# Kernel tuning notes

Hardware: AMD Instinct MI355X
Metric: run time of the kernel (lower is better)

## Reference

```python
import jax, jax.numpy as jnp
import numpy as np

LSH_NUM_PROJS = 7
BLOCK_SIZE = 256      # key block size
SAMPLE_SIZE = 256
B, H, N, D = 1, 32, 8192, 128


def _gray_perm(num_projs):
    # AngularLSH._unit_hamming_distance_array: Gray-code bucket permutation
    a = np.array([0, 1], dtype=np.int32)
    for _ in range(num_projs - 1):
        a = np.concatenate([a, np.flip(a) + a.shape[0]])
    return jnp.asarray(a)


def _lsh_hash(x, proj_dir, perm):
    # x: [B,H,N,D], proj_dir: [D,R] -> bucket ids [B,H,N]
    bits = jnp.einsum('bhnd,dr->bhnr', x, proj_dir) > 0
    enc = 2 ** jnp.arange(proj_dir.shape[-1], dtype=jnp.int32)
    bin_ids = jnp.sum(bits.astype(jnp.int32) * enc, axis=-1)
    return perm[bin_ids]


def _attn_lse(q, k, v, scale, bias=None):
    # exact attention returning output and log-sum-exp of scaled scores
    s = jnp.einsum('...qd,...kd->...qk', q, k) * scale
    if bias is not None:
        s = s + bias
    m = jnp.max(s, axis=-1, keepdims=True)
    p = jnp.exp(s - m)
    denom = jnp.sum(p, axis=-1, keepdims=True)
    attn = jnp.einsum('...qk,...kd->...qd', p, v) / denom
    lse = m + jnp.log(denom)  # [..., q, 1]
    return attn, lse


def _take(x, idx):
    # gather along the sequence axis (dim 2); idx: [B,H,M]
    return jnp.take_along_axis(x, idx[..., None], axis=2)


def hyper_attention(q, k, v, proj_dir, sampled_set):
    b, h, n, d = q.shape
    scale = d ** -0.5
    perm = _gray_perm(LSH_NUM_PROJS)
    # 1) sortLSH: sort q and k by angular-LSH bucket (stable)
    q_idx = jnp.argsort(_lsh_hash(q, proj_dir, perm), axis=2)
    k_idx = jnp.argsort(_lsh_hash(k, proj_dir, perm), axis=2)
    q_idx_inv = jnp.argsort(q_idx, axis=2)
    q_s = _take(q, q_idx)
    k_s = _take(k, k_idx)
    v_s = _take(v, k_idx)
    nb = n // BLOCK_SIZE          # number of key blocks
    qbs = n // nb                 # query block size
    # block-diagonal exact attention in sorted order
    qb = q_s.reshape(b, h, nb, qbs, d)
    kb = k_s.reshape(b, h, nb, BLOCK_SIZE, d)
    vb = v_s.reshape(b, h, nb, BLOCK_SIZE, d)
    attn_blk, lse_blk = _attn_lse(qb, kb, vb, scale)
    attn_blk = attn_blk.reshape(b, h, n, d)
    lse_blk = lse_blk.reshape(b, h, n, 1)
    attn_blk = _take(attn_blk, q_idx_inv)
    lse_blk = _take(lse_blk, q_idx_inv)
    # 2) residual: uniform sampling of keys (indices into sorted key order)
    s_size = sampled_set.shape[-1]
    k_sub = _take(k_s, sampled_set)   # [B,H,S,D]
    v_sub = _take(v_s, sampled_set)
    # mask out samples falling in the query's own diagonal block
    same_block = (jnp.arange(n)[None, None, :, None] // qbs) == (sampled_set[:, :, None, :] // BLOCK_SIZE)
    bias = jnp.where(same_block, jnp.finfo(q.dtype).min, 0.0).astype(q.dtype)
    attn_res, lse_res = _attn_lse(q_s, k_sub, v_sub, scale, bias=bias)
    lse_res = lse_res + jnp.log(n / s_size)  # importance weight n_key/sample_size
    attn_res = _take(attn_res, q_idx_inv)
    lse_res = _take(lse_res, q_idx_inv)
    # 3) combine estimators: softmax-weighted average in log space
    lse = jnp.logaddexp(lse_blk, lse_res)
    return jnp.exp(lse_blk - lse) * attn_blk + jnp.exp(lse_res - lse) * attn_res


def setup_inputs() -> dict:
    key = jax.random.key(0)
    k1, k2, k3, k4, k5 = jax.random.split(key, 5)
    return {
        'queries': jax.random.normal(k1, (B, H, N, D), dtype=jnp.float32),
        'keys': jax.random.normal(k2, (B, H, N, D), dtype=jnp.float32),
        'vals': jax.random.normal(k3, (B, H, N, D), dtype=jnp.float32),
        'proj_dir': jax.random.normal(k4, (D, LSH_NUM_PROJS), dtype=jnp.float32),
        'sampled_set': jax.random.randint(k5, (B, H, SAMPLE_SIZE), 0, N),
    }


def reference(queries, keys, vals, proj_dir, sampled_set):
    return hyper_attention(queries, keys, vals, proj_dir, sampled_set)
```

## Files before the change

kernel.cpp:

```cpp
#include <hip/hip_runtime.h>
#include <hip/hip_bf16.h>
#include <math.h>

#define Hh 32
#define Nseq 8192
#define Dh 128
#define NBd 32
#define BLKSZ 256
#define SAMP 256
#define CHK 64
#define LOG32 3.4657359027997265f
#define SCALE 0.088388347648318447f
#define SKW 136
#define SVB 264

typedef float f32x4 __attribute__((ext_vector_type(4)));
typedef unsigned ui32x4 __attribute__((ext_vector_type(4)));
typedef __bf16 bf16x8 __attribute__((ext_vector_type(8)));

__device__ __forceinline__ f32x4 mfma16(bf16x8 a, bf16x8 b, f32x4 c) {
  return __builtin_amdgcn_mfma_f32_16x16x32_bf16(a, b, c, 0, 0, 0);
}

__device__ __forceinline__ bf16x8 cvt8(const float* __restrict__ p) {
  float4 a = ((const float4*)p)[0];
  float4 b = ((const float4*)p)[1];
  bf16x8 r;
  r[0] = (__bf16)a.x; r[1] = (__bf16)a.y; r[2] = (__bf16)a.z; r[3] = (__bf16)a.w;
  r[4] = (__bf16)b.x; r[5] = (__bf16)b.y; r[6] = (__bf16)b.z; r[7] = (__bf16)b.w;
  return r;
}

__device__ __forceinline__ bf16x8 cvt8v(float4 a, float4 b) {
  bf16x8 r;
  r[0] = (__bf16)a.x; r[1] = (__bf16)a.y; r[2] = (__bf16)a.z; r[3] = (__bf16)a.w;
  r[4] = (__bf16)b.x; r[5] = (__bf16)b.y; r[6] = (__bf16)b.z; r[7] = (__bf16)b.w;
  return r;
}

__device__ __forceinline__ unsigned pack2(float a, float b, float& ra, float& rb) {
  __bf16 ba = (__bf16)a, bb = (__bf16)b;
  ra = (float)ba; rb = (float)bb;
  return ((unsigned)__builtin_bit_cast(unsigned short, bb) << 16) |
         (unsigned)__builtin_bit_cast(unsigned short, ba);
}

__global__ __launch_bounds__(256) void lsh_hash_kernel(
    const float* __restrict__ q, const float* __restrict__ k,
    const float* __restrict__ proj, int* __restrict__ buckets) {
  int row = blockIdx.x * 256 + threadIdx.x;
  const float* x = ((row >> 18) ? k : q) + (size_t)(row & (Hh * Nseq - 1)) * Dh;
  double acc[7] = {0, 0, 0, 0, 0, 0, 0};
#pragma unroll 8
  for (int d0 = 0; d0 < Dh; d0 += 4) {
    float4 xv = *(const float4*)(x + d0);
    double x0 = (double)xv.x, x1 = (double)xv.y, x2 = (double)xv.z, x3 = (double)xv.w;
#pragma unroll
    for (int j = 0; j < 7; j++) {
      acc[j] = fma(x0, (double)proj[(d0 + 0) * 7 + j], acc[j]);
      acc[j] = fma(x1, (double)proj[(d0 + 1) * 7 + j], acc[j]);
      acc[j] = fma(x2, (double)proj[(d0 + 2) * 7 + j], acc[j]);
      acc[j] = fma(x3, (double)proj[(d0 + 3) * 7 + j], acc[j]);
    }
  }
  int bin = 0;
#pragma unroll
  for (int j = 0; j < 7; j++) bin |= (acc[j] > 0.0 ? 1 : 0) << j;
  buckets[row] = bin ^ (bin >> 1);
}

__global__ __launch_bounds__(64) void bucket_sort_kernel(
    const int* __restrict__ buckets, int* __restrict__ idx) {
  __shared__ unsigned hist[64][128];
  int t = threadIdx.x;
  int base = blockIdx.x * Nseq;
  for (int b = 0; b < 128; b++) hist[t][b] = 0;
  __syncthreads();
  for (int i = 0; i < 128; i++) {
    int b = buckets[base + t * 128 + i];
    hist[t][b]++;
  }
  __syncthreads();
  int b0 = 2 * t, b1 = 2 * t + 1;
  unsigned tot0 = 0, tot1 = 0;
  for (int tt = 0; tt < 64; tt++) { unsigned h = hist[tt][b0]; hist[tt][b0] = tot0; tot0 += h; }
  for (int tt = 0; tt < 64; tt++) { unsigned h = hist[tt][b1]; hist[tt][b1] = tot1; tot1 += h; }
  unsigned pair = tot0 + tot1;
  unsigned scan = pair;
  for (int s = 1; s < 64; s <<= 1) {
    unsigned u = __shfl_up(scan, s);
    if (t >= s) scan += u;
  }
  unsigned start0 = scan - pair;
  unsigned start1 = start0 + tot0;
  __syncthreads();
  for (int tt = 0; tt < 64; tt++) { hist[tt][b0] += start0; hist[tt][b1] += start1; }
  __syncthreads();
  for (int i = 0; i < 128; i++) {
    int gi = t * 128 + i;
    int b = buckets[base + gi];
    unsigned pos = hist[t][b]++;
    idx[base + pos] = gi;
  }
}

__global__ __launch_bounds__(512, 2) void hyper_attn_blk_kernel(
    const float* __restrict__ q, const float* __restrict__ k, const float* __restrict__ v,
    const int* __restrict__ q_idx, const int* __restrict__ k_idx,
    float* __restrict__ out, float* __restrict__ lse_ws) {
  __shared__ int s_orig[BLKSZ];
  __shared__ __attribute__((aligned(16))) __bf16 s_k[2][CHK][SKW];
  __shared__ __attribute__((aligned(16))) __bf16 s_vt[2][Dh][72];

  const int c = blockIdx.x, bh = blockIdx.y;
  const int tid = threadIdx.x;
  const int w = tid >> 6, l = tid & 63;
  const int l4 = l >> 4, lm = l & 15;
  const int jk = tid >> 3, pk = tid & 7;

  if (tid < BLKSZ) s_orig[tid] = k_idx[bh * Nseq + c * BLKSZ + tid];

  bf16x8 qf[2][4];
  const int* qi = q_idx + bh * Nseq + c * BLKSZ + w * 32;
#pragma unroll
  for (int rt = 0; rt < 2; rt++) {
    int orig = qi[rt * 16 + lm];
    const float* qp = q + ((size_t)bh * Nseq + orig) * Dh + l4 * 8;
#pragma unroll
    for (int dc = 0; dc < 4; dc++) qf[rt][dc] = cvt8(qp + dc * 32);
  }

  f32x4 O[2][8];
  float mrow[2] = {-INFINITY, -INFINITY};
  float lsum[2] = {0.f, 0.f};
#pragma unroll
  for (int rt = 0; rt < 2; rt++)
#pragma unroll
    for (int dt = 0; dt < 8; dt++) { O[rt][dt][0]=0.f; O[rt][dt][1]=0.f; O[rt][dt][2]=0.f; O[rt][dt][3]=0.f; }

  __syncthreads();

  {
    int origk = s_orig[jk];
    const float* kp = k + ((size_t)bh * Nseq + origk) * Dh + pk * 16;
    *(bf16x8*)&s_k[0][jk][pk * 16]     = cvt8(kp);
    *(bf16x8*)&s_k[0][jk][pk * 16 + 8] = cvt8(kp + 8);
    int origv = s_orig[l];
    const float* vp = v + ((size_t)bh * Nseq + origv) * Dh + w * 16;
    float4 A = ((const float4*)vp)[0], B = ((const float4*)vp)[1];
    float4 C = ((const float4*)vp)[2], Dv = ((const float4*)vp)[3];
    float tmp[16] = {A.x,A.y,A.z,A.w,B.x,B.y,B.z,B.w,C.x,C.y,C.z,C.w,Dv.x,Dv.y,Dv.z,Dv.w};
#pragma unroll
    for (int dd = 0; dd < 16; dd++) s_vt[0][w * 16 + dd][l] = (__bf16)tmp[dd];
  }
  __syncthreads();

  const int laneA = lm + 32 * (l4 & 1);
  const bool hi = (l4 >> 1) & 1;

  for (int ch = 0; ch < 4; ch++) {
    const int cur = ch & 1;
    const bool pf = (ch + 1 < 4);

    float4 kA, kB, kC, kD, vA, vB, vC, vD;
    if (pf) {
      int origk = s_orig[(ch + 1) * CHK + jk];
      const float4* kp = (const float4*)(k + ((size_t)bh * Nseq + origk) * Dh + pk * 16);
      kA = kp[0]; kB = kp[1]; kC = kp[2]; kD = kp[3];
      int origv = s_orig[(ch + 1) * CHK + l];
      const float4* vp = (const float4*)(v + ((size_t)bh * Nseq + origv) * Dh + w * 16);
      vA = vp[0]; vB = vp[1]; vC = vp[2]; vD = vp[3];
    }

    float sc[2][4][4];
#pragma unroll
    for (int ct = 0; ct < 4; ct++) {
      f32x4 acc0, acc1;
      acc0[0]=0.f;acc0[1]=0.f;acc0[2]=0.f;acc0[3]=0.f;
      acc1[0]=0.f;acc1[1]=0.f;acc1[2]=0.f;acc1[3]=0.f;
#pragma unroll
      for (int dc = 0; dc < 4; dc++) {
        bf16x8 kf = *(const bf16x8*)&s_k[cur][ct * 16 + lm][dc * 32 + l4 * 8];
        acc0 = mfma16(kf, qf[0][dc], acc0);
        acc1 = mfma16(kf, qf[1][dc], acc1);
      }
#pragma unroll
      for (int r = 0; r < 4; r++) {
        sc[0][ct][r] = acc0[r] * SCALE;
        sc[1][ct][r] = acc1[r] * SCALE;
      }
    }

    unsigned q01[2][4], q23[2][4];
#pragma unroll
    for (int rt = 0; rt < 2; rt++) {
      float mc = sc[rt][0][0];
#pragma unroll
      for (int ct = 0; ct < 4; ct++)
#pragma unroll
        for (int r = 0; r < 4; r++) mc = fmaxf(mc, sc[rt][ct][r]);
      mc = fmaxf(mc, __shfl_xor(mc, 16));
      mc = fmaxf(mc, __shfl_xor(mc, 32));
      float mn = fmaxf(mrow[rt], mc);
      float alpha = __expf(mrow[rt] - mn);
      mrow[rt] = mn;
      f32x4 aO;
#pragma unroll
      for (int r = 0; r < 4; r++) aO[r] = __shfl(alpha, l4 * 4 + r);
#pragma unroll
      for (int dt = 0; dt < 8; dt++) O[rt][dt] *= aO;
      float rsum = 0.f;
#pragma unroll
      for (int ct = 0; ct < 4; ct++) {
        float p0 = __expf(sc[rt][ct][0] - mn);
        float p1 = __expf(sc[rt][ct][1] - mn);
        float p2 = __expf(sc[rt][ct][2] - mn);
        float p3 = __expf(sc[rt][ct][3] - mn);
        float ra, rb, rc, rd;
        q01[rt][ct] = pack2(p0, p1, ra, rb);
        q23[rt][ct] = pack2(p2, p3, rc, rd);
        rsum += (ra + rb) + (rc + rd);
      }
      rsum += __shfl_xor(rsum, 16);
      rsum += __shfl_xor(rsum, 32);
      lsum[rt] = lsum[rt] * alpha + rsum;
    }

    if (pf) {
      *(bf16x8*)&s_k[cur ^ 1][jk][pk * 16]     = cvt8v(kA, kB);
      *(bf16x8*)&s_k[cur ^ 1][jk][pk * 16 + 8] = cvt8v(kC, kD);
      float ta[16] = {vA.x,vA.y,vA.z,vA.w,vB.x,vB.y,vB.z,vB.w,
                      vC.x,vC.y,vC.z,vC.w,vD.x,vD.y,vD.z,vD.w};
#pragma unroll
      for (int dd = 0; dd < 16; dd++) s_vt[cur ^ 1][w * 16 + dd][l] = (__bf16)ta[dd];
    }

#pragma unroll
    for (int kc = 0; kc < 2; kc++) {
      bf16x8 pa[2];
#pragma unroll
      for (int rt = 0; rt < 2; rt++) {
        unsigned a0 = __shfl((int)q01[rt][2 * kc],     laneA);
        unsigned b0 = __shfl((int)q01[rt][2 * kc + 1], laneA);
        unsigned a1 = __shfl((int)q23[rt][2 * kc],     laneA);
        unsigned b1 = __shfl((int)q23[rt][2 * kc + 1], laneA);
        unsigned a2 = __shfl((int)q01[rt][2 * kc],     laneA + 16);
        unsigned b2 = __shfl((int)q01[rt][2 * kc + 1], laneA + 16);
        unsigned a3 = __shfl((int)q23[rt][2 * kc],     laneA + 16);
        unsigned b3 = __shfl((int)q23[rt][2 * kc + 1], laneA + 16);
        ui32x4 pw;
        pw[0] = hi ? b0 : a0;
        pw[1] = hi ? b1 : a1;
        pw[2] = hi ? b2 : a2;
        pw[3] = hi ? b3 : a3;
        pa[rt] = __builtin_bit_cast(bf16x8, pw);
      }
#pragma unroll
      for (int dt = 0; dt < 8; dt++) {
        bf16x8 vb = *(const bf16x8*)&s_vt[cur][dt * 16 + lm][kc * 32 + l4 * 8];
        O[0][dt] = mfma16(pa[0], vb, O[0][dt]);
        O[1][dt] = mfma16(pa[1], vb, O[1][dt]);
      }
    }
    __syncthreads();
  }

#pragma unroll
  for (int rt = 0; rt < 2; rt++) {
    float inv = 1.0f / lsum[rt];
    f32x4 invr;
#pragma unroll
    for (int r = 0; r < 4; r++) invr[r] = __shfl(inv, l4 * 4 + r);
    int orow[4];
#pragma unroll
    for (int r = 0; r < 4; r++)
      orow[r] = q_idx[bh * Nseq + c * BLKSZ + w * 32 + rt * 16 + l4 * 4 + r];
#pragma unroll
    for (int r = 0; r < 4; r++) {
      float* op = out + ((size_t)bh * Nseq + orow[r]) * Dh + lm;
#pragma unroll
      for (int dt = 0; dt < 8; dt++) op[dt * 16] = O[rt][dt][r] * invr[r];
    }
    if (l4 == 0) {
      int orow0 = q_idx[bh * Nseq + c * BLKSZ + w * 32 + rt * 16 + lm];
      lse_ws[bh * Nseq + orow0] = mrow[rt] + __logf(lsum[rt]);
    }
  }
}

__global__ __launch_bounds__(512, 1) void hyper_attn_res_kernel(
    const float* __restrict__ q, const float* __restrict__ k, const float* __restrict__ v,
    const int* __restrict__ sampled, const int* __restrict__ q_idx,
    const int* __restrict__ k_idx, const float* __restrict__ lse_ws,
    float* __restrict__ out) {
  __shared__ int s_sp[SAMP];
  __shared__ __attribute__((aligned(16))) __bf16 s_k[SAMP][SKW];
  __shared__ __attribute__((aligned(16))) __bf16 s_vt[Dh][SVB];

  const int bh = blockIdx.x >> 3, oct = blockIdx.x & 7;
  const int tid = threadIdx.x;
  const int w = tid >> 6, l = tid & 63;
  const int l4 = l >> 4, lm = l & 15;
  const int jk = tid >> 3, pk = tid & 7;

  if (tid < SAMP) s_sp[tid] = sampled[bh * SAMP + tid];

#pragma unroll
  for (int ps = 0; ps < 4; ps++) {
    int key = ps * 64 + jk;
    int sp = sampled[bh * SAMP + key];
    int orig = k_idx[bh * Nseq + sp];
    const float4* kp = (const float4*)(k + ((size_t)bh * Nseq + orig) * Dh + pk * 16);
    *(bf16x8*)&s_k[key][pk * 16]     = cvt8v(kp[0], kp[1]);
    *(bf16x8*)&s_k[key][pk * 16 + 8] = cvt8v(kp[2], kp[3]);
  }
#pragma unroll
  for (int ps = 0; ps < 4; ps++) {
    int key = ps * 64 + l;
    int sp = sampled[bh * SAMP + key];
    int orig = k_idx[bh * Nseq + sp];
    const float4* vp = (const float4*)(v + ((size_t)bh * Nseq + orig) * Dh + w * 16);
    float4 A = vp[0], B = vp[1], C = vp[2], Dv = vp[3];
    float tmp[16] = {A.x,A.y,A.z,A.w,B.x,B.y,B.z,B.w,C.x,C.y,C.z,C.w,Dv.x,Dv.y,Dv.z,Dv.w};
#pragma unroll
    for (int dd = 0; dd < 16; dd++) s_vt[w * 16 + dd][key] = (__bf16)tmp[dd];
  }
  __syncthreads();

  const int laneA = lm + 32 * (l4 & 1);
  const bool hi = (l4 >> 1) & 1;

  for (int t = 0; t < 4; t++) {
    const int rowb = oct * 1024 + w * 128 + t * 32;
    const int c_tile = rowb >> 8;

    bf16x8 qf[2][4];
#pragma unroll
    for (int rt = 0; rt < 2; rt++) {
      int orig = q_idx[bh * Nseq + rowb + rt * 16 + lm];
      const float* qp = q + ((size_t)bh * Nseq + orig) * Dh + l4 * 8;
#pragma unroll
      for (int dc = 0; dc < 4; dc++) qf[rt][dc] = cvt8(qp + dc * 32);
    }

    f32x4 O[2][8];
    float mrow[2] = {-INFINITY, -INFINITY};
    float lsum[2] = {0.f, 0.f};
#pragma unroll
    for (int rt = 0; rt < 2; rt++)
#pragma unroll
      for (int dt = 0; dt < 8; dt++) { O[rt][dt][0]=0.f; O[rt][dt][1]=0.f; O[rt][dt][2]=0.f; O[rt][dt][3]=0.f; }

    for (int ch = 0; ch < 4; ch++) {
      float sc[2][4][4];
#pragma unroll
      for (int ct = 0; ct < 4; ct++) {
        f32x4 acc0, acc1;
        acc0[0]=0.f;acc0[1]=0.f;acc0[2]=0.f;acc0[3]=0.f;
        acc1[0]=0.f;acc1[1]=0.f;acc1[2]=0.f;acc1[3]=0.f;
#pragma unroll
        for (int dc = 0; dc < 4; dc++) {
          bf16x8 kf = *(const bf16x8*)&s_k[ch * 64 + ct * 16 + lm][dc * 32 + l4 * 8];
          acc0 = mfma16(kf, qf[0][dc], acc0);
          acc1 = mfma16(kf, qf[1][dc], acc1);
        }
        ui32x4 spv = *(const ui32x4*)&s_sp[ch * 64 + ct * 16 + l4 * 4];
#pragma unroll
        for (int r = 0; r < 4; r++) {
          float add = ((((int)spv[r]) >> 8) == c_tile) ? -1e38f : LOG32;
          sc[0][ct][r] = acc0[r] * SCALE + add;
          sc[1][ct][r] = acc1[r] * SCALE + add;
        }
      }

      unsigned q01[2][4], q23[2][4];
#pragma unroll
      for (int rt = 0; rt < 2; rt++) {
        float mc = sc[rt][0][0];
#pragma unroll
        for (int ct = 0; ct < 4; ct++)
#pragma unroll
          for (int r = 0; r < 4; r++) mc = fmaxf(mc, sc[rt][ct][r]);
        mc = fmaxf(mc, __shfl_xor(mc, 16));
        mc = fmaxf(mc, __shfl_xor(mc, 32));
        float mn = fmaxf(mrow[rt], mc);
        float alpha = __expf(mrow[rt] - mn);
        mrow[rt] = mn;
        f32x4 aO;
#pragma unroll
        for (int r = 0; r < 4; r++) aO[r] = __shfl(alpha, l4 * 4 + r);
#pragma unroll
        for (int dt = 0; dt < 8; dt++) O[rt][dt] *= aO;
        float rsum = 0.f;
#pragma unroll
        for (int ct = 0; ct < 4; ct++) {
          float p0 = __expf(sc[rt][ct][0] - mn);
          float p1 = __expf(sc[rt][ct][1] - mn);
          float p2 = __expf(sc[rt][ct][2] - mn);
          float p3 = __expf(sc[rt][ct][3] - mn);
          float ra, rb, rc, rd;
          q01[rt][ct] = pack2(p0, p1, ra, rb);
          q23[rt][ct] = pack2(p2, p3, rc, rd);
          rsum += (ra + rb) + (rc + rd);
        }
        rsum += __shfl_xor(rsum, 16);
        rsum += __shfl_xor(rsum, 32);
        lsum[rt] = lsum[rt] * alpha + rsum;
      }

#pragma unroll
      for (int kc = 0; kc < 2; kc++) {
        bf16x8 pa[2];
#pragma unroll
        for (int rt = 0; rt < 2; rt++) {
          unsigned a0 = __shfl((int)q01[rt][2 * kc],     laneA);
          unsigned b0 = __shfl((int)q01[rt][2 * kc + 1], laneA);
          unsigned a1 = __shfl((int)q23[rt][2 * kc],     laneA);
          unsigned b1 = __shfl((int)q23[rt][2 * kc + 1], laneA);
          unsigned a2 = __shfl((int)q01[rt][2 * kc],     laneA + 16);
          unsigned b2 = __shfl((int)q01[rt][2 * kc + 1], laneA + 16);
          unsigned a3 = __shfl((int)q23[rt][2 * kc],     laneA + 16);
          unsigned b3 = __shfl((int)q23[rt][2 * kc + 1], laneA + 16);
          ui32x4 pw;
          pw[0] = hi ? b0 : a0;
          pw[1] = hi ? b1 : a1;
          pw[2] = hi ? b2 : a2;
          pw[3] = hi ? b3 : a3;
          pa[rt] = __builtin_bit_cast(bf16x8, pw);
        }
#pragma unroll
        for (int dt = 0; dt < 8; dt++) {
          bf16x8 vb = *(const bf16x8*)&s_vt[dt * 16 + lm][ch * 64 + kc * 32 + l4 * 8];
          O[0][dt] = mfma16(pa[0], vb, O[0][dt]);
          O[1][dt] = mfma16(pa[1], vb, O[1][dt]);
        }
      }
    }

#pragma unroll
    for (int rt = 0; rt < 2; rt++) {
      float lse_r = mrow[rt] + __logf(lsum[rt]);
      float inv = 1.0f / lsum[rt];
#pragma unroll
      for (int r = 0; r < 4; r++) {
        float lrr  = __shfl(lse_r, l4 * 4 + r);
        float invr = __shfl(inv,   l4 * 4 + r);
        int orow = q_idx[bh * Nseq + rowb + rt * 16 + l4 * 4 + r];
        float lb = lse_ws[bh * Nseq + orow];
        float m2 = fmaxf(lb, lrr);
        float wb = __expf(lb - m2), wr = __expf(lrr - m2);
        float sw = 1.0f / (wb + wr);
        wb *= sw; wr *= sw;
        float* op = out + ((size_t)bh * Nseq + orow) * Dh + lm;
#pragma unroll
        for (int dt = 0; dt < 8; dt++)
          op[dt * 16] = wb * op[dt * 16] + wr * (O[rt][dt][r] * invr);
      }
    }
  }
}

extern "C" void kernel_launch(void* const* d_in, const int* in_sizes, int n_in,
                              void* d_out, int out_size, void* d_ws, size_t ws_size,
                              hipStream_t stream) {
  const float* q    = (const float*)d_in[0];
  const float* k    = (const float*)d_in[1];
  const float* v    = (const float*)d_in[2];
  const float* proj = (const float*)d_in[3];
  const int* samp   = (const int*)d_in[4];
  float* out = (float*)d_out;

  int* buckets = (int*)d_ws;
  int* idx = buckets + 2 * Hh * Nseq;
  float* lse_ws = (float*)buckets;

  lsh_hash_kernel<<<(2 * Hh * Nseq) / 256, 256, 0, stream>>>(q, k, proj, buckets);
  bucket_sort_kernel<<<2 * Hh, 64, 0, stream>>>(buckets, idx);
  hyper_attn_blk_kernel<<<dim3(NBd, Hh), 512, 0, stream>>>(
      q, k, v, idx , idx + Hh * Nseq , out, lse_ws);
  hyper_attn_res_kernel<<<8 * Hh, 512, 0, stream>>>(
      q, k, v, samp, idx , idx + Hh * Nseq , lse_ws, out);
}
```

Measured before the change: 326.3 us.

## Fuse block and residual attention into one pass over 512 keys with pre-permuted bf16 K/V

Merges the block-diagonal and sampled-residual attention into one online-softmax pass per query block. Each pass covers the 256 block keys plus the 256 sampled keys, with an additive bias applying the same-block mask and the log importance weight. This removes the LSE workspace, the second kernel and the read-modify-write combine of the output. A new permute kernel writes sorted K and transposed V (and the sampled subsets) as bf16 so the attention loop does contiguous 16-byte loads without gathers or conversion. The cost is an extra pass over K/V and more workspace, with a fallback gather kernel if the workspace is too small. The sampled K/V are also no longer reused across query tiles.

Result: no change. 324.4 us (-0.6%).

```diff
diff --git a/kernel.cpp b/kernel.cpp
--- a/kernel.cpp
+++ b/kernel.cpp
@@ -8,11 +8,13 @@
 #define NBd 32
 #define BLKSZ 256
 #define SAMP 256
+#define KVT 512
 #define CHK 64
+#define NCH 8
 #define LOG32 3.4657359027997265f
 #define SCALE 0.088388347648318447f
 #define SKW 136
-#define SVB 264
+#define SVW 72
 
 typedef float f32x4 __attribute__((ext_vector_type(4)));
 typedef unsigned ui32x4 __attribute__((ext_vector_type(4)));
@@ -104,21 +106,74 @@
   }
 }
 
-__global__ __launch_bounds__(512, 2) void hyper_attn_blk_kernel(
-    const float* __restrict__ q, const float* __restrict__ k, const float* __restrict__ v,
-    const int* __restrict__ q_idx, const int* __restrict__ k_idx,
-    float* __restrict__ out, float* __restrict__ lse_ws) {
-  __shared__ int s_orig[BLKSZ];
+__global__ __launch_bounds__(256) void permute_kernel(
+    const float* __restrict__ k, const float* __restrict__ v,
+    const int* __restrict__ k_idx, const int* __restrict__ sampled,
+    __bf16* __restrict__ K_s, __bf16* __restrict__ V_t,
+    __bf16* __restrict__ K_sp, __bf16* __restrict__ V_sp) {
+  __shared__ __attribute__((aligned(16))) __bf16 s_t[Dh][SVW];
+  const int tile = blockIdx.x, bh = blockIdx.y;
+  const int t = threadIdx.x;
+  const int j = t >> 2, seg = (t & 3) * 32;
+  const bool blk = (tile < 128);
+  int dpos, orig;
+  if (blk) {
+    dpos = tile * 64 + j;
+    orig = k_idx[bh * Nseq + dpos];
+  } else {
+    dpos = (tile - 128) * 64 + j;
+    int sp = sampled[bh * SAMP + dpos];
+    orig = k_idx[bh * Nseq + sp];
+  }
+  {
+    const float4* kp = (const float4*)(k + ((size_t)bh * Nseq + orig) * Dh + seg);
+    __bf16* dst = blk ? K_s + ((size_t)bh * Nseq + dpos) * Dh + seg
+                      : K_sp + ((size_t)bh * SAMP + dpos) * Dh + seg;
+#pragma unroll
+    for (int i = 0; i < 4; i++) *(bf16x8*)(dst + i * 8) = cvt8v(kp[2 * i], kp[2 * i + 1]);
+  }
+  {
+    const float4* vp = (const float4*)(v + ((size_t)bh * Nseq + orig) * Dh + seg);
+#pragma unroll
+    for (int i = 0; i < 8; i++) {
+      float4 a = vp[i];
+      s_t[seg + i * 4 + 0][j] = (__bf16)a.x;
+      s_t[seg + i * 4 + 1][j] = (__bf16)a.y;
+      s_t[seg + i * 4 + 2][j] = (__bf16)a.z;
+      s_t[seg + i * 4 + 3][j] = (__bf16)a.w;
+    }
+  }
+  __syncthreads();
+  {
+    int d = t >> 1, half = (t & 1) * 32;
+    __bf16* dst = blk ? V_t + ((size_t)(bh * Dh + d)) * Nseq + tile * 64 + half
+                      : V_sp + ((size_t)(bh * Dh + d)) * SAMP + (tile - 128) * 64 + half;
+    const __bf16* srcp = &s_t[d][half];
+#pragma unroll
+    for (int i = 0; i < 4; i++) *(ui32x4*)(dst + i * 8) = *(const ui32x4*)(srcp + i * 8);
+  }
+}
+
+__global__ __launch_bounds__(512, 2) void hyper_attn_kernel(
+    const float* __restrict__ q, const __bf16* __restrict__ K_s,
+    const __bf16* __restrict__ V_t, const __bf16* __restrict__ K_sp,
+    const __bf16* __restrict__ V_sp, const int* __restrict__ sampled,
+    const int* __restrict__ q_idx, float* __restrict__ out) {
+  __shared__ __attribute__((aligned(16))) float s_add[SAMP];
   __shared__ __attribute__((aligned(16))) __bf16 s_k[2][CHK][SKW];
-  __shared__ __attribute__((aligned(16))) __bf16 s_vt[2][Dh][72];
+  __shared__ __attribute__((aligned(16))) __bf16 s_vt[2][Dh][SVW];
 
   const int c = blockIdx.x, bh = blockIdx.y;
   const int tid = threadIdx.x;
   const int w = tid >> 6, l = tid & 63;
   const int l4 = l >> 4, lm = l & 15;
   const int jk = tid >> 3, pk = tid & 7;
-
-  if (tid < BLKSZ) s_orig[tid] = k_idx[bh * Nseq + c * BLKSZ + tid];
+  const int dv = tid >> 2, ks = (tid & 3) * 16;
+
+  if (tid < SAMP) {
+    int sp = sampled[bh * SAMP + tid];
+    s_add[tid] = ((sp >> 8) == c) ? -1e38f : LOG32;
+  }
 
   bf16x8 qf[2][4];
   const int* qi = q_idx + bh * Nseq + c * BLKSZ + w * 32;
@@ -141,35 +196,33 @@
   __syncthreads();
 
   {
-    int origk = s_orig[jk];
-    const float* kp = k + ((size_t)bh * Nseq + origk) * Dh + pk * 16;
-    *(bf16x8*)&s_k[0][jk][pk * 16]     = cvt8(kp);
-    *(bf16x8*)&s_k[0][jk][pk * 16 + 8] = cvt8(kp + 8);
-    int origv = s_orig[l];
-    const float* vp = v + ((size_t)bh * Nseq + origv) * Dh + w * 16;
-    float4 A = ((const float4*)vp)[0], B = ((const float4*)vp)[1];
-    float4 C = ((const float4*)vp)[2], Dv = ((const float4*)vp)[3];
-    float tmp[16] = {A.x,A.y,A.z,A.w,B.x,B.y,B.z,B.w,C.x,C.y,C.z,C.w,Dv.x,Dv.y,Dv.z,Dv.w};
-#pragma unroll
-    for (int dd = 0; dd < 16; dd++) s_vt[0][w * 16 + dd][l] = (__bf16)tmp[dd];
+    const __bf16* kp = K_s + ((size_t)(bh * Nseq + c * BLKSZ) + jk) * Dh + pk * 16;
+    *(ui32x4*)&s_k[0][jk][pk * 16]     = *(const ui32x4*)kp;
+    *(ui32x4*)&s_k[0][jk][pk * 16 + 8] = *(const ui32x4*)(kp + 8);
+    const __bf16* vp = V_t + ((size_t)(bh * Dh + dv)) * Nseq + c * BLKSZ + ks;
+    *(ui32x4*)&s_vt[0][dv][ks]     = *(const ui32x4*)vp;
+    *(ui32x4*)&s_vt[0][dv][ks + 8] = *(const ui32x4*)(vp + 8);
   }
   __syncthreads();
 
   const int laneA = lm + 32 * (l4 & 1);
   const bool hi = (l4 >> 1) & 1;
 
-  for (int ch = 0; ch < 4; ch++) {
+  for (int ch = 0; ch < NCH; ch++) {
     const int cur = ch & 1;
-    const bool pf = (ch + 1 < 4);
-
-    float4 kA, kB, kC, kD, vA, vB, vC, vD;
+    const bool pf = (ch + 1 < NCH);
+
+    ui32x4 kA, kB, vA, vB;
     if (pf) {
-      int origk = s_orig[(ch + 1) * CHK + jk];
-      const float4* kp = (const float4*)(k + ((size_t)bh * Nseq + origk) * Dh + pk * 16);
-      kA = kp[0]; kB = kp[1]; kC = kp[2]; kD = kp[3];
-      int origv = s_orig[(ch + 1) * CHK + l];
-      const float4* vp = (const float4*)(v + ((size_t)bh * Nseq + origv) * Dh + w * 16);
-      vA = vp[0]; vB = vp[1]; vC = vp[2]; vD = vp[3];
+      int cn = ch + 1;
+      const __bf16* kp = (cn < 4)
+          ? K_s + ((size_t)(bh * Nseq + c * BLKSZ + cn * CHK) + jk) * Dh + pk * 16
+          : K_sp + ((size_t)(bh * SAMP + (cn - 4) * CHK) + jk) * Dh + pk * 16;
+      kA = *(const ui32x4*)kp; kB = *(const ui32x4*)(kp + 8);
+      const __bf16* vp = (cn < 4)
+          ? V_t + ((size_t)(bh * Dh + dv)) * Nseq + c * BLKSZ + cn * CHK + ks
+          : V_sp + ((size_t)(bh * Dh + dv)) * SAMP + (cn - 4) * CHK + ks;
+      vA = *(const ui32x4*)vp; vB = *(const ui32x4*)(vp + 8);
     }
 
     float sc[2][4][4];
@@ -184,10 +237,13 @@
         acc0 = mfma16(kf, qf[0][dc], acc0);
         acc1 = mfma16(kf, qf[1][dc], acc1);
       }
+      f32x4 addv;
+      if (ch < 4) { addv[0]=0.f; addv[1]=0.f; addv[2]=0.f; addv[3]=0.f; }
+      else addv = *(const f32x4*)&s_add[(ch - 4) * CHK + ct * 16 + l4 * 4];
 #pragma unroll
       for (int r = 0; r < 4; r++) {
-        sc[0][ct][r] = acc0[r] * SCALE;
-        sc[1][ct][r] = acc1[r] * SCALE;
+        sc[0][ct][r] = acc0[r] * SCALE + addv[r];
+        sc[1][ct][r] = acc1[r] * SCALE + addv[r];
       }
     }
 
@@ -227,12 +283,10 @@
     }
 
     if (pf) {
-      *(bf16x8*)&s_k[cur ^ 1][jk][pk * 16]     = cvt8v(kA, kB);
-      *(bf16x8*)&s_k[cur ^ 1][jk][pk * 16 + 8] = cvt8v(kC, kD);
-      float ta[16] = {vA.x,vA.y,vA.z,vA.w,vB.x,vB.y,vB.z,vB.w,
-                      vC.x,vC.y,vC.z,vC.w,vD.x,vD.y,vD.z,vD.w};
-#pragma unroll
-      for (int dd = 0; dd < 16; dd++) s_vt[cur ^ 1][w * 16 + dd][l] = (__bf16)ta[dd];
+      *(ui32x4*)&s_k[cur ^ 1][jk][pk * 16]     = kA;
+      *(ui32x4*)&s_k[cur ^ 1][jk][pk * 16 + 8] = kB;
+      *(ui32x4*)&s_vt[cur ^ 1][dv][ks]     = vA;
+      *(ui32x4*)&s_vt[cur ^ 1][dv][ks + 8] = vB;
     }
 
 #pragma unroll
@@ -271,191 +325,201 @@
     f32x4 invr;
 #pragma unroll
     for (int r = 0; r < 4; r++) invr[r] = __shfl(inv, l4 * 4 + r);
-    int orow[4];
-#pragma unroll
-    for (int r = 0; r < 4; r++)
-      orow[r] = q_idx[bh * Nseq + c * BLKSZ + w * 32 + rt * 16 + l4 * 4 + r];
 #pragma unroll
     for (int r = 0; r < 4; r++) {
-      float* op = out + ((size_t)bh * Nseq + orow[r]) * Dh + lm;
+      int orow = q_idx[bh * Nseq + c * BLKSZ + w * 32 + rt * 16 + l4 * 4 + r];
+      float* op = out + ((size_t)bh * Nseq + orow) * Dh + lm;
 #pragma unroll
       for (int dt = 0; dt < 8; dt++) op[dt * 16] = O[rt][dt][r] * invr[r];
     }
-    if (l4 == 0) {
-      int orow0 = q_idx[bh * Nseq + c * BLKSZ + w * 32 + rt * 16 + lm];
-      lse_ws[bh * Nseq + orow0] = mrow[rt] + __logf(lsum[rt]);
-    }
-  }
-}
-
-__global__ __launch_bounds__(512, 1) void hyper_attn_res_kernel(
+  }
+}
+
+__global__ __launch_bounds__(512, 2) void hyper_attn_fb_kernel(
     const float* __restrict__ q, const float* __restrict__ k, const float* __restrict__ v,
     const int* __restrict__ sampled, const int* __restrict__ q_idx,
-    const int* __restrict__ k_idx, const float* __restrict__ lse_ws,
-    float* __restrict__ out) {
-  __shared__ int s_sp[SAMP];
-  __shared__ __attribute__((aligned(16))) __bf16 s_k[SAMP][SKW];
-  __shared__ __attribute__((aligned(16))) __bf16 s_vt[Dh][SVB];
-
-  const int bh = blockIdx.x >> 3, oct = blockIdx.x & 7;
+    const int* __restrict__ k_idx, float* __restrict__ out) {
+  __shared__ int s_orig[KVT];
+  __shared__ __attribute__((aligned(16))) float s_addf[KVT];
+  __shared__ __attribute__((aligned(16))) __bf16 s_k[2][CHK][SKW];
+  __shared__ __attribute__((aligned(16))) __bf16 s_vt[2][Dh][SVW];
+
+  const int c = blockIdx.x, bh = blockIdx.y;
   const int tid = threadIdx.x;
   const int w = tid >> 6, l = tid & 63;
   const int l4 = l >> 4, lm = l & 15;
   const int jk = tid >> 3, pk = tid & 7;
 
-  if (tid < SAMP) s_sp[tid] = sampled[bh * SAMP + tid];
-
-#pragma unroll
-  for (int ps = 0; ps < 4; ps++) {
-    int key = ps * 64 + jk;
-    int sp = sampled[bh * SAMP + key];
-    int orig = k_idx[bh * Nseq + sp];
-    const float4* kp = (const float4*)(k + ((size_t)bh * Nseq + orig) * Dh + pk * 16);
-    *(bf16x8*)&s_k[key][pk * 16]     = cvt8v(kp[0], kp[1]);
-    *(bf16x8*)&s_k[key][pk * 16 + 8] = cvt8v(kp[2], kp[3]);
-  }
-#pragma unroll
-  for (int ps = 0; ps < 4; ps++) {
-    int key = ps * 64 + l;
-    int sp = sampled[bh * SAMP + key];
-    int orig = k_idx[bh * Nseq + sp];
-    const float4* vp = (const float4*)(v + ((size_t)bh * Nseq + orig) * Dh + w * 16);
-    float4 A = vp[0], B = vp[1], C = vp[2], Dv = vp[3];
+  {
+    int jj = tid;
+    if (jj < BLKSZ) {
+      s_orig[jj] = k_idx[bh * Nseq + c * BLKSZ + jj];
+      s_addf[jj] = 0.0f;
+    } else {
+      int sp = sampled[bh * SAMP + (jj - BLKSZ)];
+      s_orig[jj] = k_idx[bh * Nseq + sp];
+      s_addf[jj] = ((sp >> 8) == c) ? -1e38f : LOG32;
+    }
+  }
+
+  bf16x8 qf[2][4];
+  const int* qi = q_idx + bh * Nseq + c * BLKSZ + w * 32;
+#pragma unroll
+  for (int rt = 0; rt < 2; rt++) {
+    int orig = qi[rt * 16 + lm];
+    const float* qp = q + ((size_t)bh * Nseq + orig) * Dh + l4 * 8;
+#pragma unroll
+    for (int dc = 0; dc < 4; dc++) qf[rt][dc] = cvt8(qp + dc * 32);
+  }
+
+  f32x4 O[2][8];
+  float mrow[2] = {-INFINITY, -INFINITY};
+  float lsum[2] = {0.f, 0.f};
+#pragma unroll
+  for (int rt = 0; rt < 2; rt++)
+#pragma unroll
+    for (int dt = 0; dt < 8; dt++) { O[rt][dt][0]=0.f; O[rt][dt][1]=0.f; O[rt][dt][2]=0.f; O[rt][dt][3]=0.f; }
+
+  __syncthreads();
+
+  {
+    int origk = s_orig[jk];
+    const float* kp = k + ((size_t)bh * Nseq + origk) * Dh + pk * 16;
+    *(bf16x8*)&s_k[0][jk][pk * 16]     = cvt8(kp);
+    *(bf16x8*)&s_k[0][jk][pk * 16 + 8] = cvt8(kp + 8);
+    int origv = s_orig[l];
+    const float* vp = v + ((size_t)bh * Nseq + origv) * Dh + w * 16;
+    float4 A = ((const float4*)vp)[0], B = ((const float4*)vp)[1];
+    float4 C = ((const float4*)vp)[2], Dv = ((const float4*)vp)[3];
     float tmp[16] = {A.x,A.y,A.z,A.w,B.x,B.y,B.z,B.w,C.x,C.y,C.z,C.w,Dv.x,Dv.y,Dv.z,Dv.w};
 #pragma unroll
-    for (int dd = 0; dd < 16; dd++) s_vt[w * 16 + dd][key] = (__bf16)tmp[dd];
+    for (int dd = 0; dd < 16; dd++) s_vt[0][w * 16 + dd][l] = (__bf16)tmp[dd];
   }
   __syncthreads();
 
   const int laneA = lm + 32 * (l4 & 1);
   const bool hi = (l4 >> 1) & 1;
 
-  for (int t = 0; t < 4; t++) {
-    const int rowb = oct * 1024 + w * 128 + t * 32;
-    const int c_tile = rowb >> 8;
-
-    bf16x8 qf[2][4];
+  for (int ch = 0; ch < NCH; ch++) {
+    const int cur = ch & 1;
+    const bool pf = (ch + 1 < NCH);
+
+    float4 kA, kB, kC, kD, vA, vB, vC, vD;
+    if (pf) {
+      int origk = s_orig[(ch + 1) * CHK + jk];
+      const float4* kp = (const float4*)(k + ((size_t)bh * Nseq + origk) * Dh + pk * 16);
+      kA = kp[0]; kB = kp[1]; kC = kp[2]; kD = kp[3];
+      int origv = s_orig[(ch + 1) * CHK + l];
+      const float4* vp = (const float4*)(v + ((size_t)bh * Nseq + origv) * Dh + w * 16);
+      vA = vp[0]; vB = vp[1]; vC = vp[2]; vD = vp[3];
+    }
+
+    float sc[2][4][4];
+#pragma unroll
+    for (int ct = 0; ct < 4; ct++) {
+      f32x4 acc0, acc1;
+      acc0[0]=0.f;acc0[1]=0.f;acc0[2]=0.f;acc0[3]=0.f;
+      acc1[0]=0.f;acc1[1]=0.f;acc1[2]=0.f;acc1[3]=0.f;
+#pragma unroll
+      for (int dc = 0; dc < 4; dc++) {
+        bf16x8 kf = *(const bf16x8*)&s_k[cur][ct * 16 + lm][dc * 32 + l4 * 8];
+        acc0 = mfma16(kf, qf[0][dc], acc0);
+        acc1 = mfma16(kf, qf[1][dc], acc1);
+      }
+      f32x4 addv = *(const f32x4*)&s_addf[ch * CHK + ct * 16 + l4 * 4];
+#pragma unroll
+      for (int r = 0; r < 4; r++) {
+        sc[0][ct][r] = acc0[r] * SCALE + addv[r];
+        sc[1][ct][r] = acc1[r] * SCALE + addv[r];
+      }
+    }
+
+    unsigned q01[2][4], q23[2][4];
 #pragma unroll
     for (int rt = 0; rt < 2; rt++) {
-      int orig = q_idx[bh * Nseq + rowb + rt * 16 + lm];
-      const float* qp = q + ((size_t)bh * Nseq + orig) * Dh + l4 * 8;
-#pragma unroll
-      for (int dc = 0; dc < 4; dc++) qf[rt][dc] = cvt8(qp + dc * 32);
-    }
-
-    f32x4 O[2][8];
-    float mrow[2] = {-INFINITY, -INFINITY};
-    float lsum[2] = {0.f, 0.f};
-#pragma unroll
-    for (int rt = 0; rt < 2; rt++)
-#pragma unroll
-      for (int dt = 0; dt < 8; dt++) { O[rt][dt][0]=0.f; O[rt][dt][1]=0.f; O[rt][dt][2]=0.f; O[rt][dt][3]=0.f; }
-
-    for (int ch = 0; ch < 4; ch++) {
-      float sc[2][4][4];
+      float mc = sc[rt][0][0];
+#pragma unroll
+      for (int ct = 0; ct < 4; ct++)
+#pragma unroll
+        for (int r = 0; r < 4; r++) mc = fmaxf(mc, sc[rt][ct][r]);
+      mc = fmaxf(mc, __shfl_xor(mc, 16));
+      mc = fmaxf(mc, __shfl_xor(mc, 32));
+      float mn = fmaxf(mrow[rt], mc);
+      float alpha = __expf(mrow[rt] - mn);
+      mrow[rt] = mn;
+      f32x4 aO;
+#pragma unroll
+      for (int r = 0; r < 4; r++) aO[r] = __shfl(alpha, l4 * 4 + r);
+#pragma unroll
+      for (int dt = 0; dt < 8; dt++) O[rt][dt] *= aO;
+      float rsum = 0.f;
 #pragma unroll
       for (int ct = 0; ct < 4; ct++) {
-        f32x4 acc0, acc1;
-        acc0[0]=0.f;acc0[1]=0.f;acc0[2]=0.f;acc0[3]=0.f;
-        acc1[0]=0.f;acc1[1]=0.f;acc1[2]=0.f;acc1[3]=0.f;
-#pragma unroll
-        for (int dc = 0; dc < 4; dc++) {
-          bf16x8 kf = *(const bf16x8*)&s_k[ch * 64 + ct * 16 + lm][dc * 32 + l4 * 8];
-          acc0 = mfma16(kf, qf[0][dc], acc0);
-          acc1 = mfma16(kf, qf[1][dc], acc1);
-        }
-        ui32x4 spv = *(const ui32x4*)&s_sp[ch * 64 + ct * 16 + l4 * 4];
-#pragma unroll
-        for (int r = 0; r < 4; r++) {
-          float add = ((((int)spv[r]) >> 8) == c_tile) ? -1e38f : LOG32;
-          sc[0][ct][r] = acc0[r] * SCALE + add;
-          sc[1][ct][r] = acc1[r] * SCALE + add;
-        }
-      }
-
-      unsigned q01[2][4], q23[2][4];
+        float p0 = __expf(sc[rt][ct][0] - mn);
+        float p1 = __expf(sc[rt][ct][1] - mn);
+        float p2 = __expf(sc[rt][ct][2] - mn);
+        float p3 = __expf(sc[rt][ct][3] - mn);
+        float ra, rb, rc, rd;
+        q01[rt][ct] = pack2(p0, p1, ra, rb);
+        q23[rt][ct] = pack2(p2, p3, rc, rd);
+        rsum += (ra + rb) + (rc + rd);
+      }
+      rsum += __shfl_xor(rsum, 16);
+      rsum += __shfl_xor(rsum, 32);
+      lsum[rt] = lsum[rt] * alpha + rsum;
+    }
+
+    if (pf) {
+      *(bf16x8*)&s_k[cur ^ 1][jk][pk * 16]     = cvt8v(kA, kB);
+      *(bf16x8*)&s_k[cur ^ 1][jk][pk * 16 + 8] = cvt8v(kC, kD);
+      float ta[16] = {vA.x,vA.y,vA.z,vA.w,vB.x,vB.y,vB.z,vB.w,
+                      vC.x,vC.y,vC.z,vC.w,vD.x,vD.y,vD.z,vD.w};
+#pragma unroll
+      for (int dd = 0; dd < 16; dd++) s_vt[cur ^ 1][w * 16 + dd][l] = (__bf16)ta[dd];
+    }
+
+#pragma unroll
+    for (int kc = 0; kc < 2; kc++) {
+      bf16x8 pa[2];
 #pragma unroll
       for (int rt = 0; rt < 2; rt++) {
-        float mc = sc[rt][0][0];
-#pragma unroll
-        for (int ct = 0; ct < 4; ct++)
-#pragma unroll
-          for (int r = 0; r < 4; r++) mc = fmaxf(mc, sc[rt][ct][r]);
-        mc = fmaxf(mc, __shfl_xor(mc, 16));
-        mc = fmaxf(mc, __shfl_xor(mc, 32));
-        float mn = fmaxf(mrow[rt], mc);
-        float alpha = __expf(mrow[rt] - mn);
-        mrow[rt] = mn;
-        f32x4 aO;
-#pragma unroll
-        for (int r = 0; r < 4; r++) aO[r] = __shfl(alpha, l4 * 4 + r);
-#pragma unroll
-        for (int dt = 0; dt < 8; dt++) O[rt][dt] *= aO;
-        float rsum = 0.f;
-#pragma unroll
-        for (int ct = 0; ct < 4; ct++) {
-          float p0 = __expf(sc[rt][ct][0] - mn);
-          float p1 = __expf(sc[rt][ct][1] - mn);
-          float p2 = __expf(sc[rt][ct][2] - mn);
-          float p3 = __expf(sc[rt][ct][3] - mn);
-          float ra, rb, rc, rd;
-          q01[rt][ct] = pack2(p0, p1, ra, rb);
-          q23[rt][ct] = pack2(p2, p3, rc, rd);
-          rsum += (ra + rb) + (rc + rd);
-        }
-        rsum += __shfl_xor(rsum, 16);
-        rsum += __shfl_xor(rsum, 32);
-        lsum[rt] = lsum[rt] * alpha + rsum;
-      }
-
-#pragma unroll
-      for (int kc = 0; kc < 2; kc++) {
-        bf16x8 pa[2];
-#pragma unroll
-        for (int rt = 0; rt < 2; rt++) {
-          unsigned a0 = __shfl((int)q01[rt][2 * kc],     laneA);
-          unsigned b0 = __shfl((int)q01[rt][2 * kc + 1], laneA);
-          unsigned a1 = __shfl((int)q23[rt][2 * kc],     laneA);
-          unsigned b1 = __shfl((int)q23[rt][2 * kc + 1], laneA);
-          unsigned a2 = __shfl((int)q01[rt][2 * kc],     laneA + 16);
-          unsigned b2 = __shfl((int)q01[rt][2 * kc + 1], laneA + 16);
-          unsigned a3 = __shfl((int)q23[rt][2 * kc],     laneA + 16);
-          unsigned b3 = __shfl((int)q23[rt][2 * kc + 1], laneA + 16);
-          ui32x4 pw;
-          pw[0] = hi ? b0 : a0;
-          pw[1] = hi ? b1 : a1;
-          pw[2] = hi ? b2 : a2;
-          pw[3] = hi ? b3 : a3;
-          pa[rt] = __builtin_bit_cast(bf16x8, pw);
-        }
-#pragma unroll
-        for (int dt = 0; dt < 8; dt++) {
-          bf16x8 vb = *(const bf16x8*)&s_vt[dt * 16 + lm][ch * 64 + kc * 32 + l4 * 8];
-          O[0][dt] = mfma16(pa[0], vb, O[0][dt]);
-          O[1][dt] = mfma16(pa[1], vb, O[1][dt]);
-        }
-      }
-    }
-
-#pragma unroll
-    for (int rt = 0; rt < 2; rt++) {
-      float lse_r = mrow[rt] + __logf(lsum[rt]);
-      float inv = 1.0f / lsum[rt];
-#pragma unroll
-      for (int r = 0; r < 4; r++) {
-        float lrr  = __shfl(lse_r, l4 * 4 + r);
-        float invr = __shfl(inv,   l4 * 4 + r);
-        int orow = q_idx[bh * Nseq + rowb + rt * 16 + l4 * 4 + r];
-        float lb = lse_ws[bh * Nseq + orow];
-        float m2 = fmaxf(lb, lrr);
-        float wb = __expf(lb - m2), wr = __expf(lrr - m2);
-        float sw = 1.0f / (wb + wr);
-        wb *= sw; wr *= sw;
-        float* op = out + ((size_t)bh * Nseq + orow) * Dh + lm;
-#pragma unroll
-        for (int dt = 0; dt < 8; dt++)
-          op[dt * 16] = wb * op[dt * 16] + wr * (O[rt][dt][r] * invr);
-      }
+        unsigned a0 = __shfl((int)q01[rt][2 * kc],     laneA);
+        unsigned b0 = __shfl((int)q01[rt][2 * kc + 1], laneA);
+        unsigned a1 = __shfl((int)q23[rt][2 * kc],     laneA);
+        unsigned b1 = __shfl((int)q23[rt][2 * kc + 1], laneA);
+        unsigned a2 = __shfl((int)q01[rt][2 * kc],     laneA + 16);
+        unsigned b2 = __shfl((int)q01[rt][2 * kc + 1], laneA + 16);
+        unsigned a3 = __shfl((int)q23[rt][2 * kc],     laneA + 16);
+        unsigned b3 = __shfl((int)q23[rt][2 * kc + 1], laneA + 16);
+        ui32x4 pw;
+        pw[0] = hi ? b0 : a0;
+        pw[1] = hi ? b1 : a1;
+        pw[2] = hi ? b2 : a2;
+        pw[3] = hi ? b3 : a3;
+        pa[rt] = __builtin_bit_cast(bf16x8, pw);
+      }
+#pragma unroll
+      for (int dt = 0; dt < 8; dt++) {
+        bf16x8 vb = *(const bf16x8*)&s_vt[cur][dt * 16 + lm][kc * 32 + l4 * 8];
+        O[0][dt] = mfma16(pa[0], vb, O[0][dt]);
+        O[1][dt] = mfma16(pa[1], vb, O[1][dt]);
+      }
+    }
+    __syncthreads();
+  }
+
+#pragma unroll
+  for (int rt = 0; rt < 2; rt++) {
+    float inv = 1.0f / lsum[rt];
+    f32x4 invr;
+#pragma unroll
+    for (int r = 0; r < 4; r++) invr[r] = __shfl(inv, l4 * 4 + r);
+#pragma unroll
+    for (int r = 0; r < 4; r++) {
+      int orow = q_idx[bh * Nseq + c * BLKSZ + w * 32 + rt * 16 + l4 * 4 + r];
+      float* op = out + ((size_t)bh * Nseq + orow) * Dh + lm;
+#pragma unroll
+      for (int dt = 0; dt < 8; dt++) op[dt * 16] = O[rt][dt][r] * invr[r];
     }
   }
 }
@@ -472,12 +536,22 @@
 
   int* buckets = (int*)d_ws;
   int* idx = buckets + 2 * Hh * Nseq;
-  float* lse_ws = (float*)buckets;
+  __bf16* K_s  = (__bf16*)(idx + 2 * Hh * Nseq);
+  __bf16* V_t  = K_s + (size_t)Hh * Nseq * Dh;
+  __bf16* K_sp = V_t + (size_t)Hh * Nseq * Dh;
+  __bf16* V_sp = K_sp + (size_t)Hh * SAMP * Dh;
+  size_t need = (size_t)(4 * Hh * Nseq) * 4 +
+                (size_t)(2 * Hh * Nseq * Dh + 2 * Hh * SAMP * Dh) * 2;
 
   lsh_hash_kernel<<<(2 * Hh * Nseq) / 256, 256, 0, stream>>>(q, k, proj, buckets);
   bucket_sort_kernel<<<2 * Hh, 64, 0, stream>>>(buckets, idx);
-  hyper_attn_blk_kernel<<<dim3(NBd, Hh), 512, 0, stream>>>(
-      q, k, v, idx , idx + Hh * Nseq , out, lse_ws);
-  hyper_attn_res_kernel<<<8 * Hh, 512, 0, stream>>>(
-      q, k, v, samp, idx , idx + Hh * Nseq , lse_ws, out);
-}
+  if (ws_size >= need) {
+    permute_kernel<<<dim3(132, Hh), 256, 0, stream>>>(
+        k, v, idx + Hh * Nseq , samp, K_s, V_t, K_sp, V_sp);
+    hyper_attn_kernel<<<dim3(NBd, Hh), 512, 0, stream>>>(
+        q, K_s, V_t, K_sp, V_sp, samp, idx , out);
+  } else {
+    hyper_attn_fb_kernel<<<dim3(NBd, Hh), 512, 0, stream>>>(
+        q, k, v, samp, idx , idx + Hh * Nseq , out);
+  }
+}
```
